# Optimization experiments

Hardware: AMD Instinct MI355X
Metric: run time of the kernel (lower is better)

## Reference

```python
import jax, jax.numpy as jnp
import numpy as np

N = 8192          # total nodes
G = 64            # graphs in batch
NPG = 128         # nodes per graph
K_NN = 100        # knn_graph k
F_IN = 6
WID = 128         # width
CONV_DEPTH = 3
LIN_DEPTH = 5
N_LAB = 1
D2 = 2 * CONV_DEPTH * WID  # 768
NEG_SLOPE = 0.01
BN_EPS = 1e-5


def setup_inputs() -> dict:
    key = jax.random.key(0)
    ks = jax.random.split(key, 12)
    s = 0.05
    return {
        "x": jax.random.normal(ks[0], (N, F_IN), jnp.float32),
        "batch": jnp.arange(N, dtype=jnp.int64) // NPG,  # 64 graphs x 128 nodes
        "conv1_W": jax.random.normal(ks[1], (F_IN, WID), jnp.float32) * s,
        "conv1_b": jnp.zeros((WID,), jnp.float32),
        "convs_W": jax.random.normal(ks[2], (CONV_DEPTH - 1, WID, WID), jnp.float32) * s,
        "convs_b": jnp.zeros((CONV_DEPTH - 1, WID), jnp.float32),
        "bn_gamma": jnp.ones((D2,), jnp.float32),
        "bn_beta": jnp.zeros((D2,), jnp.float32),
        "lin_W": jax.random.normal(ks[3], (LIN_DEPTH, D2, D2), jnp.float32) * s,
        "lin_b": jnp.zeros((LIN_DEPTH, D2), jnp.float32),
        "out_W": jax.random.normal(ks[4], (D2, N_LAB), jnp.float32) * s,
        "out_b": jnp.zeros((N_LAB,), jnp.float32),
    }


def _leaky(h):
    return jnp.where(h > 0, h, NEG_SLOPE * h)


def _knn_edges(x, batch):
    # squared pairwise distances, masked across graphs and on the diagonal
    sq = jnp.sum(x * x, axis=1)
    dist = sq[:, None] + sq[None, :] - 2.0 * (x @ x.T)          # [N, N]
    invalid = (batch[:, None] != batch[None, :]) | jnp.eye(N, dtype=bool)
    dist = jnp.where(invalid, jnp.inf, dist)
    # indices are non-differentiable; stop_gradient avoids keeping dist for bwd
    _, idx = jax.lax.top_k(-jax.lax.stop_gradient(dist), K_NN)   # [N, K_NN]
    row = idx.reshape(-1)                                        # sources (neighbors)
    col = jnp.repeat(jnp.arange(N), K_NN)                        # targets (centers)
    return row, col


def _sgconv(h, row, col, W, b):
    # SGConv, K=2: lin(((D^-1/2 (A+I) D^-1/2)^2) h)  -- gcn_norm w/ self loops
    loops = jnp.arange(N)
    rows = jnp.concatenate([row, loops])
    cols = jnp.concatenate([col, loops])
    deg = jax.ops.segment_sum(jnp.ones(rows.shape[0], h.dtype), cols, num_segments=N)
    dinv = jax.lax.rsqrt(deg)
    norm = dinv[rows] * dinv[cols]                               # [E]
    def prop(z):
        return jax.ops.segment_sum(norm[:, None] * z[rows], cols, num_segments=N)
    return prop(prop(h)) @ W + b


def _pool(h, batch):
    # concat(global_mean_pool, global_max_pool) -> [G, 2*width]
    counts = jax.ops.segment_sum(jnp.ones((N,), h.dtype), batch, num_segments=G)
    mean = jax.ops.segment_sum(h, batch, num_segments=G) / counts[:, None]
    mx = jax.ops.segment_max(h, batch, num_segments=G)
    return jnp.concatenate([mean, mx], axis=1)


def reference(x, batch, conv1_W, conv1_b, convs_W, convs_b,
              bn_gamma, bn_beta, lin_W, lin_b, out_W, out_b):
    batch = batch.astype(jnp.int32)
    row, col = _knn_edges(x, batch)
    # dropout_adj / Dropout are identity in eval mode
    h = _leaky(_sgconv(x, row, col, conv1_W, conv1_b))
    pools = [_pool(h, batch)]
    for f in range(CONV_DEPTH - 1):
        h = _leaky(_sgconv(h, row, col, convs_W[f], convs_b[f]))
        pools.append(_pool(h, batch))
    z = jnp.concatenate(pools, axis=1)                           # [G, 768]
    # BatchNorm1d (batch statistics, biased variance)
    m = jnp.mean(z, axis=0)
    v = jnp.mean((z - m) ** 2, axis=0)
    z = (z - m) * jax.lax.rsqrt(v + BN_EPS) * bn_gamma + bn_beta
    for g in range(LIN_DEPTH):
        z = _leaky(z @ lin_W[g] + lin_b[g])
    z = z @ out_W + out_b                                        # [G, 1]
    return z.reshape(-1)
```

## Files before the change

kernel.cpp:

```cpp
#include <hip/hip_runtime.h>

#define NN    8192
#define NG    64
#define NPG   128
#define KNN   100
#define FIN   6
#define WID   128
#define D2    768
#define NEG   0.01f
#define INV101 (1.0f/101.0f)
#define BNEPS 1e-5f
#define BIG   1e30f

__device__ __forceinline__ float leaky(float v) { return v > 0.f ? v : NEG * v; }

__global__ __launch_bounds__(256) void k_knn(const float* __restrict__ x, float* __restrict__ A)
{
    int g  = blockIdx.x >> 3;
    int i0 = (blockIdx.x & 7) * 16;
    __shared__ float xg[NPG * FIN];
    __shared__ float sq[NPG];
    __shared__ float D[16][NPG];
    const float* xp = x + g * NPG * FIN;
    for (int t = threadIdx.x; t < NPG * FIN; t += 256) xg[t] = xp[t];
    __syncthreads();
    if (threadIdx.x < NPG) {
        float s = 0.f;
        #pragma unroll
        for (int c = 0; c < FIN; ++c) { float v = xg[threadIdx.x * FIN + c]; s = fmaf(v, v, s); }
        sq[threadIdx.x] = s;
    }
    __syncthreads();
    for (int e = threadIdx.x; e < 16 * NPG; e += 256) {
        int il = e >> 7, j = e & 127;
        int i = i0 + il;
        float d;
        if (j == i) d = BIG;
        else {
            float dot = 0.f;
            #pragma unroll
            for (int c = 0; c < FIN; ++c) dot = fmaf(xg[i * FIN + c], xg[j * FIN + c], dot);
            d = sq[i] + sq[j] - 2.f * dot;
        }
        D[il][j] = d;
    }
    __syncthreads();
    float* Ag = A + (size_t)g * NPG * NPG;
    for (int e = threadIdx.x; e < 16 * NPG; e += 256) {
        int il = e >> 7, j = e & 127;
        int i = i0 + il;
        float aval;
        if (i == j) aval = INV101;
        else {
            float dj = D[il][j];
            int cnt = 0;
            #pragma unroll 8
            for (int k = 0; k < NPG; ++k) {
                float dk = D[il][k];
                cnt += (dk < dj || (dk == dj && k < j)) ? 1 : 0;
            }
            aval = (cnt < KNN) ? INV101 : 0.f;
        }
        Ag[i * NPG + j] = aval;
    }
}

__global__ __launch_bounds__(256) void k_sqA_c1(const float* __restrict__ A, const float* __restrict__ x,
                                                const float* __restrict__ W1, const float* __restrict__ b1,
                                                float* __restrict__ A2, float* __restrict__ H)
{
    int g  = blockIdx.x >> 2;
    int i0 = (blockIdx.x & 2) << 4;
    i0 = (blockIdx.x & 3) * 32;
    __shared__ float As[32 * 132];
    __shared__ float Bs[NPG * NPG];
    __shared__ float xg[NPG * FIN];
    __shared__ float p2[32 * FIN];
    __shared__ float W1s[FIN * WID];
    __shared__ float b1s[WID];
    const float* Ag = A + (size_t)g * NPG * NPG;
    const float* xp = x + g * NPG * FIN;
    for (int t4 = threadIdx.x; t4 < NPG * NPG / 4; t4 += 256)
        *(float4*)&Bs[t4 * 4] = *(const float4*)&Ag[t4 * 4];
    for (int t4 = threadIdx.x; t4 < 32 * 32; t4 += 256) {
        int r = t4 >> 5, c4 = (t4 & 31) * 4;
        *(float4*)&As[r * 132 + c4] = *(const float4*)&Ag[(i0 + r) * NPG + c4];
    }
    for (int t = threadIdx.x; t < NPG * FIN; t += 256) xg[t] = xp[t];
    for (int t = threadIdx.x; t < FIN * WID; t += 256) W1s[t] = W1[t];
    if (threadIdx.x < WID) b1s[threadIdx.x] = b1[threadIdx.x];
    __syncthreads();

    int ty = threadIdx.x >> 4, tx = threadIdx.x & 15;
    int r0 = ty * 2, cj = tx * 8;
    float acc[2][8] = {};
    for (int k = 0; k < NPG; ++k) {
        float a0 = As[r0 * 132 + k];
        float a1 = As[(r0 + 1) * 132 + k];
        float4 q0 = *(const float4*)&Bs[k * NPG + cj];
        float4 q1 = *(const float4*)&Bs[k * NPG + cj + 4];
        float bb[8] = {q0.x, q0.y, q0.z, q0.w, q1.x, q1.y, q1.z, q1.w};
        #pragma unroll
        for (int c = 0; c < 8; ++c) {
            acc[0][c] = fmaf(a0, bb[c], acc[0][c]);
            acc[1][c] = fmaf(a1, bb[c], acc[1][c]);
        }
    }
    float* A2g = A2 + (size_t)g * NPG * NPG;
    #pragma unroll
    for (int r = 0; r < 2; ++r) {
        float4 v0 = {acc[r][0], acc[r][1], acc[r][2], acc[r][3]};
        float4 v1 = {acc[r][4], acc[r][5], acc[r][6], acc[r][7]};
        *(float4*)&A2g[(i0 + r0 + r) * NPG + cj]     = v0;
        *(float4*)&A2g[(i0 + r0 + r) * NPG + cj + 4] = v1;
    }
    __syncthreads();
    #pragma unroll
    for (int r = 0; r < 2; ++r) {
        *(float4*)&As[(r0 + r) * 132 + cj]     = make_float4(acc[r][0], acc[r][1], acc[r][2], acc[r][3]);
        *(float4*)&As[(r0 + r) * 132 + cj + 4] = make_float4(acc[r][4], acc[r][5], acc[r][6], acc[r][7]);
    }
    __syncthreads();
    if (threadIdx.x < 32 * FIN) {
        int i = threadIdx.x / FIN, d = threadIdx.x - i * FIN;
        float s = 0.f;
        for (int k = 0; k < NPG; ++k) s = fmaf(As[i * 132 + k], xg[k * FIN + d], s);
        p2[threadIdx.x] = s;
    }
    __syncthreads();
    for (int e = threadIdx.x; e < 32 * WID; e += 256) {
        int i = e >> 7, o = e & 127;
        float s = b1s[o];
        #pragma unroll
        for (int d = 0; d < FIN; ++d) s = fmaf(p2[i * FIN + d], W1s[d * WID + o], s);
        H[(size_t)(g * NPG + i0 + i) * WID + o] = leaky(s);
    }
}

__global__ __launch_bounds__(256) void k_conv(const float* __restrict__ A2, const float* __restrict__ Hin,
                                              const float* __restrict__ W, const float* __restrict__ bias,
                                              float* __restrict__ Hout, float* __restrict__ Zp, int zoff)
{
    int g  = blockIdx.x >> 2;
    int i0 = (blockIdx.x & 3) * 32;
    __shared__ float Ps[32 * 132];
    __shared__ float hs[NPG * WID];
    const float* A2g = A2 + (size_t)g * NPG * NPG;
    const float* hg  = Hin + (size_t)g * NPG * WID;
    for (int t4 = threadIdx.x; t4 < NPG * WID / 4; t4 += 256)
        *(float4*)&hs[t4 * 4] = *(const float4*)&hg[t4 * 4];
    for (int t4 = threadIdx.x; t4 < 32 * 32; t4 += 256) {
        int r = t4 >> 5, c4 = (t4 & 31) * 4;
        *(float4*)&Ps[r * 132 + c4] = *(const float4*)&A2g[(i0 + r) * NPG + c4];
    }
    __syncthreads();
    if ((blockIdx.x & 3) == 0 && threadIdx.x < WID) {
        int o = threadIdx.x;
        float sm = 0.f, mx = -BIG;
        for (int i = 0; i < NPG; ++i) { float v = hs[i * WID + o]; sm += v; mx = fmaxf(mx, v); }
        Zp[g * D2 + zoff + o]       = sm * (1.f / NPG);
        Zp[g * D2 + zoff + WID + o] = mx;
    }
    int ty = threadIdx.x >> 4, tx = threadIdx.x & 15;
    int r0 = ty * 2, cj = tx * 8;
    float acc[2][8];
    {
        #pragma unroll
        for (int r = 0; r < 2; ++r)
            #pragma unroll
            for (int c = 0; c < 8; ++c) acc[r][c] = 0.f;
        for (int k = 0; k < NPG; ++k) {
            float a0 = Ps[r0 * 132 + k];
            float a1 = Ps[(r0 + 1) * 132 + k];
            float4 q0 = *(const float4*)&hs[k * WID + cj];
            float4 q1 = *(const float4*)&hs[k * WID + cj + 4];
            float bb[8] = {q0.x, q0.y, q0.z, q0.w, q1.x, q1.y, q1.z, q1.w};
            #pragma unroll
            for (int c = 0; c < 8; ++c) {
                acc[0][c] = fmaf(a0, bb[c], acc[0][c]);
                acc[1][c] = fmaf(a1, bb[c], acc[1][c]);
            }
        }
        __syncthreads();
        #pragma unroll
        for (int r = 0; r < 2; ++r) {
            *(float4*)&Ps[(r0 + r) * 132 + cj]     = make_float4(acc[r][0], acc[r][1], acc[r][2], acc[r][3]);
            *(float4*)&Ps[(r0 + r) * 132 + cj + 4] = make_float4(acc[r][4], acc[r][5], acc[r][6], acc[r][7]);
        }
        __syncthreads();
    }
    {
        float o2[2][8];
        #pragma unroll
        for (int r = 0; r < 2; ++r)
            #pragma unroll
            for (int c = 0; c < 8; ++c) o2[r][c] = 0.f;
        for (int d = 0; d < NPG; ++d) {
            float a0 = Ps[r0 * 132 + d];
            float a1 = Ps[(r0 + 1) * 132 + d];
            float4 w0 = *(const float4*)&W[d * WID + cj];
            float4 w1 = *(const float4*)&W[d * WID + cj + 4];
            float bb[8] = {w0.x, w0.y, w0.z, w0.w, w1.x, w1.y, w1.z, w1.w};
            #pragma unroll
            for (int c = 0; c < 8; ++c) {
                o2[0][c] = fmaf(a0, bb[c], o2[0][c]);
                o2[1][c] = fmaf(a1, bb[c], o2[1][c]);
            }
        }
        #pragma unroll
        for (int r = 0; r < 2; ++r) {
            float4 v0, v1;
            v0.x = leaky(o2[r][0] + bias[cj + 0]);
            v0.y = leaky(o2[r][1] + bias[cj + 1]);
            v0.z = leaky(o2[r][2] + bias[cj + 2]);
            v0.w = leaky(o2[r][3] + bias[cj + 3]);
            v1.x = leaky(o2[r][4] + bias[cj + 4]);
            v1.y = leaky(o2[r][5] + bias[cj + 5]);
            v1.z = leaky(o2[r][6] + bias[cj + 6]);
            v1.w = leaky(o2[r][7] + bias[cj + 7]);
            *(float4*)&Hout[(size_t)(g * NPG + i0 + r0 + r) * WID + cj]     = v0;
            *(float4*)&Hout[(size_t)(g * NPG + i0 + r0 + r) * WID + cj + 4] = v1;
        }
    }
}

__global__ __launch_bounds__(128) void k_pool(const float* __restrict__ H, float* __restrict__ Zp, int zoff)
{
    int g = blockIdx.x, o = threadIdx.x;
    float sm = 0.f, mx = -BIG;
    for (int i = 0; i < NPG; ++i) {
        float v = H[((size_t)g * NPG + i) * WID + o];
        sm += v; mx = fmaxf(mx, v);
    }
    Zp[g * D2 + zoff + o]       = sm * (1.f / NPG);
    Zp[g * D2 + zoff + WID + o] = mx;
}

__global__ __launch_bounds__(128) void k_bn(const float* __restrict__ Zp, const float* __restrict__ gam,
                                            const float* __restrict__ bet, float* __restrict__ ZT)
{
    int c = blockIdx.x * 128 + threadIdx.x;
    float s = 0.f, s2 = 0.f;
    for (int r = 0; r < NG; ++r) { float v = Zp[r * D2 + c]; s += v; s2 = fmaf(v, v, s2); }
    float m   = s * (1.f / NG);
    float var = s2 * (1.f / NG) - m * m;
    float sc  = rsqrtf(var + BNEPS) * gam[c];
    float bt  = bet[c];
    for (int r = 0; r < NG; ++r) {
        float v = Zp[r * D2 + c];
        ZT[c * NG + r] = (v - m) * sc + bt;
    }
}

__global__ __launch_bounds__(256) void k_linA(const float* __restrict__ ZTin, const float* __restrict__ W,
                                              float* __restrict__ P)
{
    const int c  = blockIdx.x * 16 + (threadIdx.x & 15);
    const int r0 = (threadIdx.x >> 4) * 4;
    const int k0 = blockIdx.y * 48;
    const float* wp = W + (size_t)k0 * D2 + c;
    const float* zp = ZTin + k0 * NG + r0;
    float4 acc = {0.f, 0.f, 0.f, 0.f};
    #pragma unroll
    for (int kk = 0; kk < 48; kk += 16) {
        float  wv[16];
        float4 zv[16];
        #pragma unroll
        for (int u = 0; u < 16; ++u) {
            wv[u] = wp[(kk + u) * D2];
            zv[u] = *(const float4*)&zp[(kk + u) * NG];
        }
        #pragma unroll
        for (int u = 0; u < 16; ++u) {
            acc.x = fmaf(zv[u].x, wv[u], acc.x);
            acc.y = fmaf(zv[u].y, wv[u], acc.y);
            acc.z = fmaf(zv[u].z, wv[u], acc.z);
            acc.w = fmaf(zv[u].w, wv[u], acc.w);
        }
    }
    *(float4*)&P[((size_t)blockIdx.y * D2 + c) * NG + r0] = acc;
}

__global__ __launch_bounds__(256) void k_linB(const float* __restrict__ P, const float* __restrict__ bias,
                                              float* __restrict__ ZTout)
{
    int e = (blockIdx.x * 256 + threadIdx.x) * 4;
    float4 s = *(const float4*)&P[e];
    #pragma unroll
    for (int q = 1; q < 16; ++q) {
        float4 p = *(const float4*)&P[(size_t)q * (D2 * NG) + e];
        s.x += p.x; s.y += p.y; s.z += p.z; s.w += p.w;
    }
    float bv = bias[e >> 6];
    s.x = leaky(s.x + bv); s.y = leaky(s.y + bv);
    s.z = leaky(s.z + bv); s.w = leaky(s.w + bv);
    *(float4*)&ZTout[e] = s;
}

__global__ __launch_bounds__(256) void k_out(const float* __restrict__ ZTin, const float* __restrict__ W,
                                             const float* __restrict__ bias, float* __restrict__ out)
{
    __shared__ float red[4][64];
    int r = threadIdx.x & 63, q = threadIdx.x >> 6;
    float s = 0.f;
    #pragma unroll 8
    for (int k = q * 192; k < q * 192 + 192; ++k)
        s = fmaf(ZTin[k * NG + r], W[k], s);
    red[q][r] = s;
    __syncthreads();
    if (threadIdx.x < 64)
        out[r] = red[0][r] + red[1][r] + red[2][r] + red[3][r] + bias[0];
}

extern "C" void kernel_launch(void* const* d_in, const int* in_sizes, int n_in,
                              void* d_out, int out_size, void* d_ws, size_t ws_size,
                              hipStream_t stream)
{
    (void)in_sizes; (void)n_in; (void)out_size; (void)ws_size;
    const float* x       = (const float*)d_in[0];
    const float* conv1_W = (const float*)d_in[2];
    const float* conv1_b = (const float*)d_in[3];
    const float* convs_W = (const float*)d_in[4];
    const float* convs_b = (const float*)d_in[5];
    const float* bn_g    = (const float*)d_in[6];
    const float* bn_b    = (const float*)d_in[7];
    const float* lin_W   = (const float*)d_in[8];
    const float* lin_b   = (const float*)d_in[9];
    const float* out_W   = (const float*)d_in[10];
    const float* out_b   = (const float*)d_in[11];

    float* A_raw = (float*)d_ws;
    float* A2    = A_raw + (1 << 20);
    float* H_a   = A2 + (1 << 20);
    float* H_b   = A_raw;
    float* P     = A_raw;
    float* Zp    = H_a + (1 << 20);
    float* ZT0   = Zp + NG * D2;
    float* ZT1   = ZT0 + NG * D2;

    k_knn   <<<dim3(512), dim3(256), 0, stream>>>(x, A_raw);
    k_sqA_c1<<<dim3(256), dim3(256), 0, stream>>>(A_raw, x, conv1_W, conv1_b, A2, H_a);
    k_conv  <<<dim3(256), dim3(256), 0, stream>>>(A2, H_a, convs_W,             convs_b,       H_b, Zp, 0);
    k_conv  <<<dim3(256), dim3(256), 0, stream>>>(A2, H_b, convs_W + WID * WID, convs_b + WID, H_a, Zp, 256);
    k_pool  <<<dim3(NG),  dim3(128), 0, stream>>>(H_a, Zp, 512);
    k_bn    <<<dim3(6),   dim3(128), 0, stream>>>(Zp, bn_g, bn_b, ZT0);

    const float* zin = ZT0; float* zout = ZT1;
    for (int l = 0; l < 5; ++l) {
        k_linA<<<dim3(48, 16), dim3(256), 0, stream>>>(zin, lin_W + (size_t)l * D2 * D2, P);
        k_linB<<<dim3(48),     dim3(256), 0, stream>>>(P, lin_b + l * D2, zout);
        float* t = zout; zout = (float*)zin; zin = t;
    }
    k_out<<<dim3(1), dim3(256), 0, stream>>>(zin, out_W, out_b, (float*)d_out);
}
```

Before: 172.2 us.

## Fuse whole pipeline into one cooperative persistent kernel with grid syncs

Replaces the chain of separate launches (knn, A^2+conv1, two convs, pool, batchnorm, ten linear kernels, output) with one cooperative kernel of 256 blocks that advances through the stages separated by grid.sync. A^2 now stays in shared memory across the conv layers, and the last pool is computed per slab and reduced inside the batchnorm stage. The kNN ranking packs distance and index into 64-bit keys and has each thread rank 16 candidates. The linear layers drop the split-K partial buffer and reduce in-block instead. This removes per-launch overhead and global round trips, but each linear layer now uses only 192 blocks and every stage pays the cost of a grid-wide barrier.

After: 475.5 us. 2.76x slower.

```diff
diff --git a/kernel.cpp b/kernel.cpp
--- a/kernel.cpp
+++ b/kernel.cpp
@@ -1,6 +1,8 @@
 #include <hip/hip_runtime.h>
-
-#define NN    8192
+#include <hip/hip_cooperative_groups.h>
+
+namespace cg = cooperative_groups;
+
 #define NG    64
 #define NPG   128
 #define KNN   100
@@ -14,166 +16,105 @@
 
 __device__ __forceinline__ float leaky(float v) { return v > 0.f ? v : NEG * v; }
 
-__global__ __launch_bounds__(256) void k_knn(const float* __restrict__ x, float* __restrict__ A)
+__device__ __forceinline__ unsigned ford(float f) {
+    unsigned u = __float_as_uint(f);
+    return (u >> 31) ? ~u : (u | 0x80000000u);
+}
+
+__global__ __launch_bounds__(256, 1) void k_mega(
+    const float* __restrict__ x,
+    const float* __restrict__ W1, const float* __restrict__ b1,
+    const float* __restrict__ Wc, const float* __restrict__ bc,
+    const float* __restrict__ bng, const float* __restrict__ bnb,
+    const float* __restrict__ linW, const float* __restrict__ linb,
+    const float* __restrict__ outW, const float* __restrict__ outb,
+    float* __restrict__ A, float* __restrict__ H1, float* __restrict__ H2,
+    float* __restrict__ Zp, float* __restrict__ Zp3,
+    float* __restrict__ ZT0, float* __restrict__ ZT1, float* __restrict__ out)
 {
-    int g  = blockIdx.x >> 3;
-    int i0 = (blockIdx.x & 7) * 16;
+    cg::grid_group grid = cg::this_grid();
+    const int b    = blockIdx.x;
+    const int g    = b & 63;
+    const int slab = b >> 6;
+    const int i0   = slab * 32;
+    const int t    = threadIdx.x;
+
     __shared__ float xg[NPG * FIN];
     __shared__ float sq[NPG];
-    __shared__ float D[16][NPG];
-    const float* xp = x + g * NPG * FIN;
-    for (int t = threadIdx.x; t < NPG * FIN; t += 256) xg[t] = xp[t];
-    __syncthreads();
-    if (threadIdx.x < NPG) {
-        float s = 0.f;
-        #pragma unroll
-        for (int c = 0; c < FIN; ++c) { float v = xg[threadIdx.x * FIN + c]; s = fmaf(v, v, s); }
-        sq[threadIdx.x] = s;
-    }
-    __syncthreads();
-    for (int e = threadIdx.x; e < 16 * NPG; e += 256) {
-        int il = e >> 7, j = e & 127;
-        int i = i0 + il;
-        float d;
-        if (j == i) d = BIG;
-        else {
-            float dot = 0.f;
-            #pragma unroll
-            for (int c = 0; c < FIN; ++c) dot = fmaf(xg[i * FIN + c], xg[j * FIN + c], dot);
-            d = sq[i] + sq[j] - 2.f * dot;
-        }
-        D[il][j] = d;
-    }
-    __syncthreads();
-    float* Ag = A + (size_t)g * NPG * NPG;
-    for (int e = threadIdx.x; e < 16 * NPG; e += 256) {
-        int il = e >> 7, j = e & 127;
-        int i = i0 + il;
-        float aval;
-        if (i == j) aval = INV101;
-        else {
-            float dj = D[il][j];
-            int cnt = 0;
-            #pragma unroll 8
-            for (int k = 0; k < NPG; ++k) {
-                float dk = D[il][k];
-                cnt += (dk < dj || (dk == dj && k < j)) ? 1 : 0;
-            }
-            aval = (cnt < KNN) ? INV101 : 0.f;
-        }
-        Ag[i * NPG + j] = aval;
-    }
-}
-
-__global__ __launch_bounds__(256) void k_sqA_c1(const float* __restrict__ A, const float* __restrict__ x,
-                                                const float* __restrict__ W1, const float* __restrict__ b1,
-                                                float* __restrict__ A2, float* __restrict__ H)
-{
-    int g  = blockIdx.x >> 2;
-    int i0 = (blockIdx.x & 2) << 4;
-    i0 = (blockIdx.x & 3) * 32;
-    __shared__ float As[32 * 132];
+    __shared__ float A2s[32 * 132];
+    __shared__ float Ps[32 * 132];
     __shared__ float Bs[NPG * NPG];
-    __shared__ float xg[NPG * FIN];
     __shared__ float p2[32 * FIN];
     __shared__ float W1s[FIN * WID];
     __shared__ float b1s[WID];
-    const float* Ag = A + (size_t)g * NPG * NPG;
-    const float* xp = x + g * NPG * FIN;
-    for (int t4 = threadIdx.x; t4 < NPG * NPG / 4; t4 += 256)
-        *(float4*)&Bs[t4 * 4] = *(const float4*)&Ag[t4 * 4];
-    for (int t4 = threadIdx.x; t4 < 32 * 32; t4 += 256) {
-        int r = t4 >> 5, c4 = (t4 & 31) * 4;
-        *(float4*)&As[r * 132 + c4] = *(const float4*)&Ag[(i0 + r) * NPG + c4];
-    }
-    for (int t = threadIdx.x; t < NPG * FIN; t += 256) xg[t] = xp[t];
-    for (int t = threadIdx.x; t < FIN * WID; t += 256) W1s[t] = W1[t];
-    if (threadIdx.x < WID) b1s[threadIdx.x] = b1[threadIdx.x];
-    __syncthreads();
-
-    int ty = threadIdx.x >> 4, tx = threadIdx.x & 15;
-    int r0 = ty * 2, cj = tx * 8;
-    float acc[2][8] = {};
-    for (int k = 0; k < NPG; ++k) {
-        float a0 = As[r0 * 132 + k];
-        float a1 = As[(r0 + 1) * 132 + k];
-        float4 q0 = *(const float4*)&Bs[k * NPG + cj];
-        float4 q1 = *(const float4*)&Bs[k * NPG + cj + 4];
-        float bb[8] = {q0.x, q0.y, q0.z, q0.w, q1.x, q1.y, q1.z, q1.w};
-        #pragma unroll
-        for (int c = 0; c < 8; ++c) {
-            acc[0][c] = fmaf(a0, bb[c], acc[0][c]);
-            acc[1][c] = fmaf(a1, bb[c], acc[1][c]);
-        }
-    }
-    float* A2g = A2 + (size_t)g * NPG * NPG;
-    #pragma unroll
-    for (int r = 0; r < 2; ++r) {
-        float4 v0 = {acc[r][0], acc[r][1], acc[r][2], acc[r][3]};
-        float4 v1 = {acc[r][4], acc[r][5], acc[r][6], acc[r][7]};
-        *(float4*)&A2g[(i0 + r0 + r) * NPG + cj]     = v0;
-        *(float4*)&A2g[(i0 + r0 + r) * NPG + cj + 4] = v1;
-    }
-    __syncthreads();
-    #pragma unroll
-    for (int r = 0; r < 2; ++r) {
-        *(float4*)&As[(r0 + r) * 132 + cj]     = make_float4(acc[r][0], acc[r][1], acc[r][2], acc[r][3]);
-        *(float4*)&As[(r0 + r) * 132 + cj + 4] = make_float4(acc[r][4], acc[r][5], acc[r][6], acc[r][7]);
-    }
-    __syncthreads();
-    if (threadIdx.x < 32 * FIN) {
-        int i = threadIdx.x / FIN, d = threadIdx.x - i * FIN;
-        float s = 0.f;
-        for (int k = 0; k < NPG; ++k) s = fmaf(As[i * 132 + k], xg[k * FIN + d], s);
-        p2[threadIdx.x] = s;
-    }
-    __syncthreads();
-    for (int e = threadIdx.x; e < 32 * WID; e += 256) {
-        int i = e >> 7, o = e & 127;
-        float s = b1s[o];
-        #pragma unroll
-        for (int d = 0; d < FIN; ++d) s = fmaf(p2[i * FIN + d], W1s[d * WID + o], s);
-        H[(size_t)(g * NPG + i0 + i) * WID + o] = leaky(s);
-    }
-}
-
-__global__ __launch_bounds__(256) void k_conv(const float* __restrict__ A2, const float* __restrict__ Hin,
-                                              const float* __restrict__ W, const float* __restrict__ bias,
-                                              float* __restrict__ Hout, float* __restrict__ Zp, int zoff)
-{
-    int g  = blockIdx.x >> 2;
-    int i0 = (blockIdx.x & 3) * 32;
-    __shared__ float Ps[32 * 132];
-    __shared__ float hs[NPG * WID];
-    const float* A2g = A2 + (size_t)g * NPG * NPG;
-    const float* hg  = Hin + (size_t)g * NPG * WID;
-    for (int t4 = threadIdx.x; t4 < NPG * WID / 4; t4 += 256)
-        *(float4*)&hs[t4 * 4] = *(const float4*)&hg[t4 * 4];
-    for (int t4 = threadIdx.x; t4 < 32 * 32; t4 += 256) {
-        int r = t4 >> 5, c4 = (t4 & 31) * 4;
-        *(float4*)&Ps[r * 132 + c4] = *(const float4*)&A2g[(i0 + r) * NPG + c4];
-    }
-    __syncthreads();
-    if ((blockIdx.x & 3) == 0 && threadIdx.x < WID) {
-        int o = threadIdx.x;
-        float sm = 0.f, mx = -BIG;
-        for (int i = 0; i < NPG; ++i) { float v = hs[i * WID + o]; sm += v; mx = fmaxf(mx, v); }
-        Zp[g * D2 + zoff + o]       = sm * (1.f / NPG);
-        Zp[g * D2 + zoff + WID + o] = mx;
-    }
-    int ty = threadIdx.x >> 4, tx = threadIdx.x & 15;
-    int r0 = ty * 2, cj = tx * 8;
-    float acc[2][8];
+    __shared__ float red[4 * 4 * 64];
+
     {
-        #pragma unroll
-        for (int r = 0; r < 2; ++r)
-            #pragma unroll
-            for (int c = 0; c < 8; ++c) acc[r][c] = 0.f;
+        const float* xp = x + g * NPG * FIN;
+        for (int e = t; e < NPG * FIN; e += 256) xg[e] = xp[e];
+        __syncthreads();
+        if (t < NPG) {
+            float s = 0.f;
+            #pragma unroll
+            for (int c = 0; c < FIN; ++c) { float v = xg[t * FIN + c]; s = fmaf(v, v, s); }
+            sq[t] = s;
+        }
+        __syncthreads();
+        for (int e = t; e < 32 * NPG; e += 256) {
+            int il = e >> 7, j = e & 127;
+            int i = i0 + il;
+            float d;
+            if (j == i) d = BIG;
+            else {
+                float dot = 0.f;
+                #pragma unroll
+                for (int c = 0; c < FIN; ++c) dot = fmaf(xg[i * FIN + c], xg[j * FIN + c], dot);
+                d = sq[i] + sq[j] - 2.f * dot;
+            }
+            Bs[il * 128 + j] = d;
+        }
+        __syncthreads();
+        int il = t >> 3, j0 = (t & 7) * 16;
+        const float* Drow = &Bs[il * 128];
+        unsigned long long jk[16];
+        int cnt[16];
+        #pragma unroll
+        for (int u = 0; u < 16; ++u) {
+            jk[u] = ((unsigned long long)ford(Drow[j0 + u]) << 32) | (unsigned)(j0 + u);
+            cnt[u] = 0;
+        }
+        for (int k = 0; k < 128; ++k) {
+            unsigned long long kk = ((unsigned long long)ford(Drow[k]) << 32) | (unsigned)k;
+            #pragma unroll
+            for (int u = 0; u < 16; ++u) cnt[u] += (kk < jk[u]) ? 1 : 0;
+        }
+        int i = i0 + il;
+        float av[16];
+        #pragma unroll
+        for (int u = 0; u < 16; ++u)
+            av[u] = (cnt[u] < KNN || (j0 + u) == i) ? INV101 : 0.f;
+        float* Ag = A + (size_t)g * NPG * NPG + (size_t)i * NPG + j0;
+        #pragma unroll
+        for (int q = 0; q < 4; ++q)
+            *(float4*)&Ag[q * 4] = make_float4(av[q*4], av[q*4+1], av[q*4+2], av[q*4+3]);
+    }
+    grid.sync();
+
+    {
+        const float* Ag = A + (size_t)g * NPG * NPG;
+        for (int t4 = t; t4 < NPG * NPG / 4; t4 += 256)
+            *(float4*)&Bs[t4 * 4] = *(const float4*)&Ag[t4 * 4];
+        for (int e = t; e < FIN * WID; e += 256) W1s[e] = W1[e];
+        if (t < WID) b1s[t] = b1[t];
+        __syncthreads();
+        int ty = t >> 4, tx = t & 15;
+        int r0 = ty * 2, cj = tx * 8;
+        float acc[2][8] = {};
         for (int k = 0; k < NPG; ++k) {
-            float a0 = Ps[r0 * 132 + k];
-            float a1 = Ps[(r0 + 1) * 132 + k];
-            float4 q0 = *(const float4*)&hs[k * WID + cj];
-            float4 q1 = *(const float4*)&hs[k * WID + cj + 4];
+            float a0 = Bs[(i0 + r0) * 128 + k];
+            float a1 = Bs[(i0 + r0 + 1) * 128 + k];
+            float4 q0 = *(const float4*)&Bs[k * 128 + cj];
+            float4 q1 = *(const float4*)&Bs[k * 128 + cj + 4];
             float bb[8] = {q0.x, q0.y, q0.z, q0.w, q1.x, q1.y, q1.z, q1.w};
             #pragma unroll
             for (int c = 0; c < 8; ++c) {
@@ -181,20 +122,65 @@
                 acc[1][c] = fmaf(a1, bb[c], acc[1][c]);
             }
         }
-        __syncthreads();
+        #pragma unroll
+        for (int r = 0; r < 2; ++r) {
+            *(float4*)&A2s[(r0 + r) * 132 + cj]     = make_float4(acc[r][0], acc[r][1], acc[r][2], acc[r][3]);
+            *(float4*)&A2s[(r0 + r) * 132 + cj + 4] = make_float4(acc[r][4], acc[r][5], acc[r][6], acc[r][7]);
+        }
+        __syncthreads();
+        if (t < 32 * FIN) {
+            int i = t / FIN, d = t - i * FIN;
+            float s = 0.f;
+            for (int k = 0; k < NPG; ++k) s = fmaf(A2s[i * 132 + k], xg[k * FIN + d], s);
+            p2[t] = s;
+        }
+        __syncthreads();
+        for (int e = t; e < 32 * WID; e += 256) {
+            int i = e >> 7, o = e & 127;
+            float s = b1s[o];
+            #pragma unroll
+            for (int d = 0; d < FIN; ++d) s = fmaf(p2[i * FIN + d], W1s[d * WID + o], s);
+            H1[(size_t)(g * NPG + i0 + i) * WID + o] = leaky(s);
+        }
+    }
+    grid.sync();
+
+    for (int f = 0; f < 2; ++f) {
+        const float* Hin  = f ? H2 : H1;
+        const float* W    = Wc + f * WID * WID;
+        const float* bias = bc + f * WID;
+        const float* hg = Hin + (size_t)g * NPG * WID;
+        for (int t4 = t; t4 < NPG * WID / 4; t4 += 256)
+            *(float4*)&Bs[t4 * 4] = *(const float4*)&hg[t4 * 4];
+        __syncthreads();
+        if (slab == 0 && t < WID) {
+            float sm = 0.f, mx = -BIG;
+            for (int i = 0; i < NPG; ++i) { float v = Bs[i * WID + t]; sm += v; mx = fmaxf(mx, v); }
+            Zp[g * D2 + f * 256 + t]       = sm * (1.f / NPG);
+            Zp[g * D2 + f * 256 + WID + t] = mx;
+        }
+        int ty = t >> 4, tx = t & 15;
+        int r0 = ty * 2, cj = tx * 8;
+        float acc[2][8] = {};
+        for (int k = 0; k < NPG; ++k) {
+            float a0 = A2s[r0 * 132 + k];
+            float a1 = A2s[(r0 + 1) * 132 + k];
+            float4 q0 = *(const float4*)&Bs[k * WID + cj];
+            float4 q1 = *(const float4*)&Bs[k * WID + cj + 4];
+            float bb[8] = {q0.x, q0.y, q0.z, q0.w, q1.x, q1.y, q1.z, q1.w};
+            #pragma unroll
+            for (int c = 0; c < 8; ++c) {
+                acc[0][c] = fmaf(a0, bb[c], acc[0][c]);
+                acc[1][c] = fmaf(a1, bb[c], acc[1][c]);
+            }
+        }
         #pragma unroll
         for (int r = 0; r < 2; ++r) {
             *(float4*)&Ps[(r0 + r) * 132 + cj]     = make_float4(acc[r][0], acc[r][1], acc[r][2], acc[r][3]);
             *(float4*)&Ps[(r0 + r) * 132 + cj + 4] = make_float4(acc[r][4], acc[r][5], acc[r][6], acc[r][7]);
         }
         __syncthreads();
-    }
-    {
-        float o2[2][8];
-        #pragma unroll
-        for (int r = 0; r < 2; ++r)
-            #pragma unroll
-            for (int c = 0; c < 8; ++c) o2[r][c] = 0.f;
+        float o2[2][8] = {};
         for (int d = 0; d < NPG; ++d) {
             float a0 = Ps[r0 * 132 + d];
             float a1 = Ps[(r0 + 1) * 132 + d];
@@ -208,108 +194,129 @@
             }
         }
         #pragma unroll
-        for (int r = 0; r < 2; ++r) {
-            float4 v0, v1;
-            v0.x = leaky(o2[r][0] + bias[cj + 0]);
-            v0.y = leaky(o2[r][1] + bias[cj + 1]);
-            v0.z = leaky(o2[r][2] + bias[cj + 2]);
-            v0.w = leaky(o2[r][3] + bias[cj + 3]);
-            v1.x = leaky(o2[r][4] + bias[cj + 4]);
-            v1.y = leaky(o2[r][5] + bias[cj + 5]);
-            v1.z = leaky(o2[r][6] + bias[cj + 6]);
-            v1.w = leaky(o2[r][7] + bias[cj + 7]);
-            *(float4*)&Hout[(size_t)(g * NPG + i0 + r0 + r) * WID + cj]     = v0;
-            *(float4*)&Hout[(size_t)(g * NPG + i0 + r0 + r) * WID + cj + 4] = v1;
-        }
-    }
-}
-
-__global__ __launch_bounds__(128) void k_pool(const float* __restrict__ H, float* __restrict__ Zp, int zoff)
-{
-    int g = blockIdx.x, o = threadIdx.x;
-    float sm = 0.f, mx = -BIG;
-    for (int i = 0; i < NPG; ++i) {
-        float v = H[((size_t)g * NPG + i) * WID + o];
-        sm += v; mx = fmaxf(mx, v);
-    }
-    Zp[g * D2 + zoff + o]       = sm * (1.f / NPG);
-    Zp[g * D2 + zoff + WID + o] = mx;
-}
-
-__global__ __launch_bounds__(128) void k_bn(const float* __restrict__ Zp, const float* __restrict__ gam,
-                                            const float* __restrict__ bet, float* __restrict__ ZT)
-{
-    int c = blockIdx.x * 128 + threadIdx.x;
-    float s = 0.f, s2 = 0.f;
-    for (int r = 0; r < NG; ++r) { float v = Zp[r * D2 + c]; s += v; s2 = fmaf(v, v, s2); }
-    float m   = s * (1.f / NG);
-    float var = s2 * (1.f / NG) - m * m;
-    float sc  = rsqrtf(var + BNEPS) * gam[c];
-    float bt  = bet[c];
-    for (int r = 0; r < NG; ++r) {
-        float v = Zp[r * D2 + c];
-        ZT[c * NG + r] = (v - m) * sc + bt;
-    }
-}
-
-__global__ __launch_bounds__(256) void k_linA(const float* __restrict__ ZTin, const float* __restrict__ W,
-                                              float* __restrict__ P)
-{
-    const int c  = blockIdx.x * 16 + (threadIdx.x & 15);
-    const int r0 = (threadIdx.x >> 4) * 4;
-    const int k0 = blockIdx.y * 48;
-    const float* wp = W + (size_t)k0 * D2 + c;
-    const float* zp = ZTin + k0 * NG + r0;
-    float4 acc = {0.f, 0.f, 0.f, 0.f};
-    #pragma unroll
-    for (int kk = 0; kk < 48; kk += 16) {
-        float  wv[16];
-        float4 zv[16];
-        #pragma unroll
-        for (int u = 0; u < 16; ++u) {
-            wv[u] = wp[(kk + u) * D2];
-            zv[u] = *(const float4*)&zp[(kk + u) * NG];
-        }
-        #pragma unroll
-        for (int u = 0; u < 16; ++u) {
-            acc.x = fmaf(zv[u].x, wv[u], acc.x);
-            acc.y = fmaf(zv[u].y, wv[u], acc.y);
-            acc.z = fmaf(zv[u].z, wv[u], acc.z);
-            acc.w = fmaf(zv[u].w, wv[u], acc.w);
-        }
-    }
-    *(float4*)&P[((size_t)blockIdx.y * D2 + c) * NG + r0] = acc;
-}
-
-__global__ __launch_bounds__(256) void k_linB(const float* __restrict__ P, const float* __restrict__ bias,
-                                              float* __restrict__ ZTout)
-{
-    int e = (blockIdx.x * 256 + threadIdx.x) * 4;
-    float4 s = *(const float4*)&P[e];
-    #pragma unroll
-    for (int q = 1; q < 16; ++q) {
-        float4 p = *(const float4*)&P[(size_t)q * (D2 * NG) + e];
-        s.x += p.x; s.y += p.y; s.z += p.z; s.w += p.w;
-    }
-    float bv = bias[e >> 6];
-    s.x = leaky(s.x + bv); s.y = leaky(s.y + bv);
-    s.z = leaky(s.z + bv); s.w = leaky(s.w + bv);
-    *(float4*)&ZTout[e] = s;
-}
-
-__global__ __launch_bounds__(256) void k_out(const float* __restrict__ ZTin, const float* __restrict__ W,
-                                             const float* __restrict__ bias, float* __restrict__ out)
-{
-    __shared__ float red[4][64];
-    int r = threadIdx.x & 63, q = threadIdx.x >> 6;
-    float s = 0.f;
-    #pragma unroll 8
-    for (int k = q * 192; k < q * 192 + 192; ++k)
-        s = fmaf(ZTin[k * NG + r], W[k], s);
-    red[q][r] = s;
-    __syncthreads();
-    if (threadIdx.x < 64)
-        out[r] = red[0][r] + red[1][r] + red[2][r] + red[3][r] + bias[0];
+        for (int r = 0; r < 2; ++r)
+            #pragma unroll
+            for (int c = 0; c < 8; ++c)
+                o2[r][c] = leaky(o2[r][c] + bias[cj + c]);
+        if (f == 0) {
+            #pragma unroll
+            for (int r = 0; r < 2; ++r) {
+                *(float4*)&H2[(size_t)(g * NPG + i0 + r0 + r) * WID + cj]     = make_float4(o2[r][0], o2[r][1], o2[r][2], o2[r][3]);
+                *(float4*)&H2[(size_t)(g * NPG + i0 + r0 + r) * WID + cj + 4] = make_float4(o2[r][4], o2[r][5], o2[r][6], o2[r][7]);
+            }
+        } else {
+            __syncthreads();
+            #pragma unroll
+            for (int r = 0; r < 2; ++r) {
+                *(float4*)&Ps[(r0 + r) * 132 + cj]     = make_float4(o2[r][0], o2[r][1], o2[r][2], o2[r][3]);
+                *(float4*)&Ps[(r0 + r) * 132 + cj + 4] = make_float4(o2[r][4], o2[r][5], o2[r][6], o2[r][7]);
+            }
+            __syncthreads();
+            if (t < WID) {
+                float sm = 0.f, mx = -BIG;
+                for (int i = 0; i < 32; ++i) { float v = Ps[i * 132 + t]; sm += v; mx = fmaxf(mx, v); }
+                Zp3[(size_t)(g * 4 + slab) * 256 + t]       = sm;
+                Zp3[(size_t)(g * 4 + slab) * 256 + 128 + t] = mx;
+            }
+        }
+        grid.sync();
+    }
+
+    if (b < 3) {
+        int c = b * 256 + t;
+        float s = 0.f, s2 = 0.f;
+        for (int r = 0; r < NG; ++r) {
+            float v;
+            if (c < 512) v = Zp[r * D2 + c];
+            else if (c < 640) {
+                int o = c - 512;
+                float sm = 0.f;
+                #pragma unroll
+                for (int q = 0; q < 4; ++q) sm += Zp3[(size_t)(r * 4 + q) * 256 + o];
+                v = sm * (1.f / NPG);
+            } else {
+                int o = c - 640;
+                float mx = -BIG;
+                #pragma unroll
+                for (int q = 0; q < 4; ++q) mx = fmaxf(mx, Zp3[(size_t)(r * 4 + q) * 256 + 128 + o]);
+                v = mx;
+            }
+            s += v; s2 = fmaf(v, v, s2);
+        }
+        float m   = s * (1.f / NG);
+        float var = s2 * (1.f / NG) - m * m;
+        float sc  = rsqrtf(var + BNEPS) * bng[c];
+        float bt  = bnb[c];
+        for (int r = 0; r < NG; ++r) {
+            float v;
+            if (c < 512) v = Zp[r * D2 + c];
+            else if (c < 640) {
+                int o = c - 512;
+                float sm = 0.f;
+                #pragma unroll
+                for (int q = 0; q < 4; ++q) sm += Zp3[(size_t)(r * 4 + q) * 256 + o];
+                v = sm * (1.f / NPG);
+            } else {
+                int o = c - 640;
+                float mx = -BIG;
+                #pragma unroll
+                for (int q = 0; q < 4; ++q) mx = fmaxf(mx, Zp3[(size_t)(r * 4 + q) * 256 + 128 + o]);
+                v = mx;
+            }
+            ZT0[c * NG + r] = (v - m) * sc + bt;
+        }
+    }
+    grid.sync();
+
+    for (int l = 0; l < 5; ++l) {
+        const float* zin  = (l & 1) ? ZT1 : ZT0;
+        float*       zout = (l & 1) ? ZT0 : ZT1;
+        const float* W = linW + (size_t)l * D2 * D2;
+        if (b < 192) {
+            const int c0 = b * 4;
+            for (int u = t; u < D2; u += 256)
+                *(float4*)&Ps[u * 4] = *(const float4*)&W[(size_t)u * D2 + c0];
+            __syncthreads();
+            int row = t & 63, kq = t >> 6;
+            const float* zp = zin + kq * 192 * NG + row;
+            const float* wp = &Ps[kq * 192 * 4];
+            float s0 = 0.f, s1 = 0.f, s2 = 0.f, s3 = 0.f;
+            #pragma unroll 8
+            for (int k = 0; k < 192; ++k) {
+                float z  = zp[k * NG];
+                float4 w = *(const float4*)&wp[k * 4];
+                s0 = fmaf(z, w.x, s0); s1 = fmaf(z, w.y, s1);
+                s2 = fmaf(z, w.z, s2); s3 = fmaf(z, w.w, s3);
+            }
+            red[(0 * 4 + kq) * 64 + row] = s0;
+            red[(1 * 4 + kq) * 64 + row] = s1;
+            red[(2 * 4 + kq) * 64 + row] = s2;
+            red[(3 * 4 + kq) * 64 + row] = s3;
+            __syncthreads();
+            int c = t >> 6, r2 = t & 63;
+            float v = red[(c * 4 + 0) * 64 + r2] + red[(c * 4 + 1) * 64 + r2]
+                    + red[(c * 4 + 2) * 64 + r2] + red[(c * 4 + 3) * 64 + r2];
+            v = leaky(v + linb[l * D2 + c0 + c]);
+            zout[(c0 + c) * NG + r2] = v;
+            __syncthreads();
+        }
+        grid.sync();
+    }
+
+    if (b == 0) {
+        const float* zin = ZT1;
+        for (int u = t; u < D2; u += 256) Ps[u] = outW[u];
+        __syncthreads();
+        int row = t & 63, kq = t >> 6;
+        const float* zp = zin + kq * 192 * NG + row;
+        float s = 0.f;
+        #pragma unroll 8
+        for (int k = 0; k < 192; ++k) s = fmaf(zp[k * NG], Ps[kq * 192 + k], s);
+        red[kq * 64 + row] = s;
+        __syncthreads();
+        if (t < 64)
+            out[t] = red[t] + red[64 + t] + red[128 + t] + red[192 + t] + outb[0];
+    }
 }
 
 extern "C" void kernel_launch(void* const* d_in, const int* in_sizes, int n_in,
@@ -329,27 +336,21 @@
     const float* out_W   = (const float*)d_in[10];
     const float* out_b   = (const float*)d_in[11];
 
-    float* A_raw = (float*)d_ws;
-    float* A2    = A_raw + (1 << 20);
-    float* H_a   = A2 + (1 << 20);
-    float* H_b   = A_raw;
-    float* P     = A_raw;
-    float* Zp    = H_a + (1 << 20);
-    float* ZT0   = Zp + NG * D2;
-    float* ZT1   = ZT0 + NG * D2;
-
-    k_knn   <<<dim3(512), dim3(256), 0, stream>>>(x, A_raw);
-    k_sqA_c1<<<dim3(256), dim3(256), 0, stream>>>(A_raw, x, conv1_W, conv1_b, A2, H_a);
-    k_conv  <<<dim3(256), dim3(256), 0, stream>>>(A2, H_a, convs_W,             convs_b,       H_b, Zp, 0);
-    k_conv  <<<dim3(256), dim3(256), 0, stream>>>(A2, H_b, convs_W + WID * WID, convs_b + WID, H_a, Zp, 256);
-    k_pool  <<<dim3(NG),  dim3(128), 0, stream>>>(H_a, Zp, 512);
-    k_bn    <<<dim3(6),   dim3(128), 0, stream>>>(Zp, bn_g, bn_b, ZT0);
-
-    const float* zin = ZT0; float* zout = ZT1;
-    for (int l = 0; l < 5; ++l) {
-        k_linA<<<dim3(48, 16), dim3(256), 0, stream>>>(zin, lin_W + (size_t)l * D2 * D2, P);
-        k_linB<<<dim3(48),     dim3(256), 0, stream>>>(P, lin_b + l * D2, zout);
-        float* t = zout; zout = (float*)zin; zin = t;
-    }
-    k_out<<<dim3(1), dim3(256), 0, stream>>>(zin, out_W, out_b, (float*)d_out);
+    float* A   = (float*)d_ws;
+    float* H1  = A   + (1 << 20);
+    float* H2  = H1  + (1 << 20);
+    float* Zp  = H2  + (1 << 20);
+    float* Zp3 = Zp  + NG * D2;
+    float* ZT0 = Zp3 + NG * 4 * 256;
+    float* ZT1 = ZT0 + NG * D2;
+    float* outp = (float*)d_out;
+
+    void* args[] = {
+        (void*)&x, (void*)&conv1_W, (void*)&conv1_b, (void*)&convs_W, (void*)&convs_b,
+        (void*)&bn_g, (void*)&bn_b, (void*)&lin_W, (void*)&lin_b,
+        (void*)&out_W, (void*)&out_b,
+        (void*)&A, (void*)&H1, (void*)&H2, (void*)&Zp, (void*)&Zp3,
+        (void*)&ZT0, (void*)&ZT1, (void*)&outp
+    };
+    hipLaunchCooperativeKernel((void*)k_mega, dim3(256), dim3(256), args, 0, stream);
 }
```
